# Kernel tuning notes

Measured on AMD Instinct MI355X. Metric: run time of the kernel, lower is better.

Reference implementation:

```python
import jax, jax.numpy as jnp
import numpy as np

H = 12
D_MODEL = 768
D_K = D_MODEL // H  # 64


def setup_inputs() -> dict:
    key = jax.random.key(0)
    ks = jax.random.split(key, 16)
    B, S, D = 4, 1024, D_MODEL
    scale = 1.0 / np.sqrt(D)
    inp = {
        "query": jax.random.normal(ks[0], (B, S, D), jnp.float32),
        "key": jax.random.normal(ks[1], (B, S, D), jnp.float32),
        "value": jax.random.normal(ks[2], (B, S, D), jnp.float32),
        "times": jax.random.normal(ks[3], (2, B, S, D), jnp.float32),
        # learned params (Linear weights stored torch-style [out, in])
        "Wq": jax.random.normal(ks[4], (D, D), jnp.float32) * scale,
        "bq": jnp.zeros((D,), jnp.float32),
        "Wk": jax.random.normal(ks[5], (D, D), jnp.float32) * scale,
        "bk": jnp.zeros((D,), jnp.float32),
        "Wv": jax.random.normal(ks[6], (D, D), jnp.float32) * scale,
        "bv": jnp.zeros((D,), jnp.float32),
        "Wt": jax.random.normal(ks[7], (D, D), jnp.float32) * scale,
        "bt": jnp.zeros((D,), jnp.float32),
        "Wo": jax.random.normal(ks[8], (D, D), jnp.float32) * scale,
        "bo": jnp.zeros((D,), jnp.float32),
    }
    return inp


def _split_heads(x, B, S):
    # [B,S,D] -> [B,H,S,D_K]
    return x.reshape(B, S, H, D_K).transpose(0, 2, 1, 3)


def reference(query, key, value, times, Wq, bq, Wk, bk, Wv, bv, Wt, bt, Wo, bo):
    B, S, D = query.shape
    inv_sqrt_dk = 1.0 / jnp.sqrt(jnp.asarray(D_K, query.dtype))
    # q/k/v projections are identical across time-loop iterations; hoist them.
    q = _split_heads(query @ Wq.T + bq, B, S)   # [B,H,S,dk]
    k = _split_heads(key @ Wk.T + bk, B, S)
    v = _split_heads(value @ Wv.T + bv, B, S)
    x = jnp.zeros_like(q)
    n_times = times.shape[0]
    for i in range(n_times):  # small fixed loop over time embeddings
        t = _split_heads(times[i] @ Wt.T + bt, B, S)
        # dual-score attention: query.time + query.key, each scaled by 1/sqrt(d_k)
        scores = (jnp.einsum('bhqd,bhkd->bhqk', q, t)
                  + jnp.einsum('bhqd,bhkd->bhqk', q, k)) * inv_sqrt_dk
        p = jax.nn.softmax(scores, axis=-1)
        x = x + jnp.einsum('bhqk,bhkd->bhqd', p, v)
    x = x.transpose(0, 2, 1, 3).reshape(B, S, H * D_K)
    return x @ Wo.T + bo
```

## Files before the change

### kernel.cpp

```cpp
#include <hip/hip_runtime.h>
#include <hip/hip_fp16.h>

typedef _Float16 v8h __attribute__((ext_vector_type(8)));
typedef _Float16 v4h __attribute__((ext_vector_type(4)));
typedef float v4f __attribute__((ext_vector_type(4)));

#define MFMA_F16 __builtin_amdgcn_mfma_f32_16x16x32_f16

__device__ static inline void async_copy16(const void* g, void* l) {
  __builtin_amdgcn_global_load_lds(
      (const __attribute__((address_space(1))) void*)g,
      (__attribute__((address_space(3))) void*)l, 16, 0, 0);
}

struct CastArgs {
  const float* src[10];
  _Float16* dst[10];
  int n8[10];
  float scale[10];
};
__global__ void cast_all(CastArgs a) {
  const int z = blockIdx.y;
  const int i = blockIdx.x * 256 + threadIdx.x;
  if (i >= a.n8[z]) return;
  const float sc = a.scale[z];
  const float* s = a.src[z] + (size_t)i * 8;
  const float4 f0 = *(const float4*)s;
  const float4 f1 = *(const float4*)(s + 4);
  v8h o = {(_Float16)(f0.x * sc), (_Float16)(f0.y * sc),
           (_Float16)(f0.z * sc), (_Float16)(f0.w * sc),
           (_Float16)(f1.x * sc), (_Float16)(f1.y * sc),
           (_Float16)(f1.z * sc), (_Float16)(f1.w * sc)};
  *(v8h*)(a.dst[z] + (size_t)i * 8) = o;
}

struct GemmArgs {
  const _Float16* A1[4]; const _Float16* A2[4];
  const _Float16* W1[4]; const _Float16* W2[4];
  const float* b1[4];    const float* b2[4];
  void* out[4];
  float bscale[4];
  int K[4];
  int mode[4];
};

__global__ __launch_bounds__(256) void gemm_mt(GemmArgs g) {
  __shared__ _Float16 a_lds[128 * 64];
  __shared__ _Float16 w_lds[128 * 64];
  const int z = blockIdx.z;
  const int KK = g.K[z];
  const int tid = threadIdx.x;
  const int w = tid >> 6, lane = tid & 63, quad = lane >> 4, l16 = lane & 15;
  const int m0 = blockIdx.x * 128, n0 = blockIdx.y * 128;
  const int wm = (w >> 1) * 64, wn = (w & 1) * 64;

  size_t srcOff[4]; int ldsOff[4];
  #pragma unroll
  for (int i = 0; i < 4; ++i) {
    const int c = i * 256 + tid, row = c >> 3, slot = c & 7;
    srcOff[i] = (size_t)row * 768 + (size_t)((slot ^ (row & 7)) * 8);
    ldsOff[i] = (i * 256 + w * 64) * 8;
  }

  v4f acc[4][4] = {};

  for (int k0 = 0; k0 < KK; k0 += 64) {
    const _Float16* Asrc = (k0 < 768) ? g.A1[z] : g.A2[z];
    const _Float16* Wsrc = (k0 < 768) ? g.W1[z] : g.W2[z];
    const int kc = (k0 < 768) ? k0 : k0 - 768;
    __syncthreads();
    #pragma unroll
    for (int i = 0; i < 4; ++i) {
      async_copy16(Asrc + (size_t)m0 * 768 + kc + srcOff[i], &a_lds[ldsOff[i]]);
      async_copy16(Wsrc + (size_t)n0 * 768 + kc + srcOff[i], &w_lds[ldsOff[i]]);
    }
    __syncthreads();

    #pragma unroll
    for (int kh = 0; kh < 2; ++kh) {
      v8h af[4], bf[4];
      #pragma unroll
      for (int mt = 0; mt < 4; ++mt) {
        const int r = wm + mt * 16 + l16;
        af[mt] = *(const v8h*)&a_lds[r * 64 + (((kh * 4 + quad) ^ (r & 7)) * 8)];
      }
      #pragma unroll
      for (int nt = 0; nt < 4; ++nt) {
        const int r = wn + nt * 16 + l16;
        bf[nt] = *(const v8h*)&w_lds[r * 64 + (((kh * 4 + quad) ^ (r & 7)) * 8)];
      }
      #pragma unroll
      for (int mt = 0; mt < 4; ++mt)
        #pragma unroll
        for (int nt = 0; nt < 4; ++nt)
          acc[mt][nt] = MFMA_F16(af[mt], bf[nt], acc[mt][nt], 0, 0, 0);
    }
  }

  const int mode = g.mode[z];
  #pragma unroll
  for (int nt = 0; nt < 4; ++nt) {
    const int col = n0 + wn + nt * 16 + l16;
    float bv = g.b1[z][col] * g.bscale[z];
    if (g.b2[z]) bv += g.b2[z][col];
    if (mode == 1) {
      _Float16* outp = (_Float16*)g.out[z];
      const int h = col >> 6, dk = col & 63;
      #pragma unroll
      for (int mt = 0; mt < 4; ++mt) {
        const int row = m0 + wm + mt * 16 + quad * 4;
        const int b = row >> 10, s = row & 1023;
        v4h pack = {(_Float16)(acc[mt][nt][0] + bv), (_Float16)(acc[mt][nt][1] + bv),
                    (_Float16)(acc[mt][nt][2] + bv), (_Float16)(acc[mt][nt][3] + bv)};
        *(v4h*)&outp[(size_t)((b * 12 + h) * 64 + dk) * 1024 + s] = pack;
      }
    } else {
      #pragma unroll
      for (int mt = 0; mt < 4; ++mt)
        #pragma unroll
        for (int r = 0; r < 4; ++r) {
          const int row = m0 + wm + mt * 16 + quad * 4 + r;
          const float v = acc[mt][nt][r] + bv;
          if (mode == 2) ((float*)g.out[z])[(size_t)row * 768 + col] = v;
          else ((_Float16*)g.out[z])[(size_t)row * 768 + col] = (_Float16)v;
        }
    }
  }
}

__global__ __launch_bounds__(128) void attn(
    const _Float16* __restrict__ Q,
    const _Float16* __restrict__ KT0, const _Float16* __restrict__ KT1,
    const _Float16* __restrict__ Vt,
    _Float16* __restrict__ X)
{
  __shared__ _Float16 kt0[2][2048];
  __shared__ _Float16 kt1[2][2048];
  __shared__ _Float16 vt[2][2048];
  __shared__ _Float16 p_lds[2][2][2][16 * 40];

  const int tid = threadIdx.x;
  const int w = tid >> 6, lane = tid & 63, quad = lane >> 4, l16 = lane & 15;
  const int bh = blockIdx.y, b = bh / 12, h = bh % 12;
  const int q0 = blockIdx.x * 64;
  const size_t base = (size_t)b * 1024 * 768 + h * 64;

  const _Float16* KT0b = KT0 + base;
  const _Float16* KT1b = KT1 + base;
  const _Float16* Vtb = Vt + (size_t)bh * 64 * 1024;

  size_t ktOff[2], vOff[2]; int ldsOff[2];
  #pragma unroll
  for (int i = 0; i < 2; ++i) {
    const int c = i * 128 + w * 64 + lane, row = c >> 3, slot = c & 7;
    const int logical = slot ^ (row & 7);
    ktOff[i] = (size_t)row * 768 + (size_t)(logical * 8);
    vOff[i] = (size_t)(row * 2 + (logical >> 2)) * 1024 + (size_t)((logical & 3) * 8);
    ldsOff[i] = c * 8;
  }
  auto stage = [&](int kv0, int buf) {
    #pragma unroll
    for (int i = 0; i < 2; ++i) {
      async_copy16(KT0b + (size_t)kv0 * 768 + ktOff[i], &kt0[buf][ldsOff[i]]);
      async_copy16(KT1b + (size_t)kv0 * 768 + ktOff[i], &kt1[buf][ldsOff[i]]);
      async_copy16(Vtb + vOff[i] + kv0, &vt[buf][ldsOff[i]]);
    }
  };

  const _Float16* Qw = Q + base + (size_t)(q0 + w * 32) * 768;
  v8h qf[2][2];
  #pragma unroll
  for (int u = 0; u < 2; ++u)
    #pragma unroll
    for (int kh = 0; kh < 2; ++kh)
      qf[u][kh] = *(const v8h*)(Qw + (size_t)(u * 16 + l16) * 768 + kh * 32 + quad * 8);

  v4f o[2][2][4] = {};
  float sm[2][2][4] = {};

  stage(0, 0);
  for (int c = 0; c < 32; ++c) {
    __syncthreads();
    if (c < 31) stage((c + 1) * 32, (c + 1) & 1);
    const _Float16* k0p = &kt0[c & 1][0];
    const _Float16* k1p = &kt1[c & 1][0];
    const _Float16* vp = &vt[c & 1][0];

    v8h bfr[2][2][2];
    #pragma unroll
    for (int kvt = 0; kvt < 2; ++kvt) {
      const int r = kvt * 16 + l16, rw = r & 7;
      bfr[0][kvt][0] = *(const v8h*)&k0p[r * 64 + ((quad ^ rw) * 8)];
      bfr[0][kvt][1] = *(const v8h*)&k0p[r * 64 + (((4 + quad) ^ rw) * 8)];
      bfr[1][kvt][0] = *(const v8h*)&k1p[r * 64 + ((quad ^ rw) * 8)];
      bfr[1][kvt][1] = *(const v8h*)&k1p[r * 64 + (((4 + quad) ^ rw) * 8)];
    }

    v4f s[2][2][2] = {};
    #pragma unroll
    for (int u = 0; u < 2; ++u)
      #pragma unroll
      for (int t = 0; t < 2; ++t)
        #pragma unroll
        for (int kvt = 0; kvt < 2; ++kvt) {
          s[u][t][kvt] = MFMA_F16(qf[u][0], bfr[t][kvt][0], s[u][t][kvt], 0, 0, 0);
          s[u][t][kvt] = MFMA_F16(qf[u][1], bfr[t][kvt][1], s[u][t][kvt], 0, 0, 0);
        }

    #pragma unroll
    for (int u = 0; u < 2; ++u)
      #pragma unroll
      for (int t = 0; t < 2; ++t) {
        _Float16* pl = &p_lds[w][u][t][0];
        #pragma unroll
        for (int r = 0; r < 4; ++r) {
          const int prow = quad * 4 + r;
          const float e0 = __expf(s[u][t][0][r]);
          const float e1 = __expf(s[u][t][1][r]);
          sm[u][t][r] += e0 + e1;
          pl[prow * 40 + l16] = (_Float16)e0;
          pl[prow * 40 + 16 + l16] = (_Float16)e1;
        }
      }
    __builtin_amdgcn_s_waitcnt(0xC07F);

    v8h pf[2][2];
    #pragma unroll
    for (int u = 0; u < 2; ++u)
      #pragma unroll
      for (int t = 0; t < 2; ++t)
        pf[u][t] = *(const v8h*)&p_lds[w][u][t][l16 * 40 + quad * 8];

    #pragma unroll
    for (int nt = 0; nt < 4; ++nt) {
      const int n = nt * 16 + l16, row = n >> 1;
      const int slot = ((n & 1) * 4 + quad) ^ (row & 7);
      const v8h vf = *(const v8h*)&vp[row * 64 + slot * 8];
      #pragma unroll
      for (int u = 0; u < 2; ++u)
        #pragma unroll
        for (int t = 0; t < 2; ++t)
          o[u][t][nt] = MFMA_F16(pf[u][t], vf, o[u][t][nt], 0, 0, 0);
    }
  }

  #pragma unroll
  for (int u = 0; u < 2; ++u) {
    _Float16* Xw = X + base + (size_t)(q0 + w * 32 + u * 16) * 768;
    #pragma unroll
    for (int r = 0; r < 4; ++r) {
      float s0 = sm[u][0][r], s1 = sm[u][1][r];
      s0 += __shfl_xor(s0, 1); s0 += __shfl_xor(s0, 2);
      s0 += __shfl_xor(s0, 4); s0 += __shfl_xor(s0, 8);
      s1 += __shfl_xor(s1, 1); s1 += __shfl_xor(s1, 2);
      s1 += __shfl_xor(s1, 4); s1 += __shfl_xor(s1, 8);
      const float i0 = 1.0f / s0, i1 = 1.0f / s1;
      #pragma unroll
      for (int nt = 0; nt < 4; ++nt)
        Xw[(size_t)(quad * 4 + r) * 768 + nt * 16 + l16] =
            (_Float16)(o[u][0][nt][r] * i0 + o[u][1][nt][r] * i1);
    }
  }
}

extern "C" void kernel_launch(void* const* d_in, const int* in_sizes, int n_in,
                              void* d_out, int out_size, void* d_ws, size_t ws_size,
                              hipStream_t stream) {
  const float* query = (const float*)d_in[0];
  const float* key   = (const float*)d_in[1];
  const float* value = (const float*)d_in[2];
  const float* times = (const float*)d_in[3];
  const float* Wq = (const float*)d_in[4];  const float* bq = (const float*)d_in[5];
  const float* Wk = (const float*)d_in[6];  const float* bk = (const float*)d_in[7];
  const float* Wv = (const float*)d_in[8];  const float* bv = (const float*)d_in[9];
  const float* Wt = (const float*)d_in[10]; const float* bt = (const float*)d_in[11];
  const float* Wo = (const float*)d_in[12]; const float* bo = (const float*)d_in[13];
  float* out = (float*)d_out;

  const size_t NELEM = (size_t)4096 * 768;
  const size_t WELEM = (size_t)768 * 768;

  char* ws = (char*)d_ws;
  size_t off = 0;
  auto alloc = [&](size_t bytes) {
    void* p = ws + off; off += (bytes + 255) & ~(size_t)255; return p;
  };
  _Float16* qh  = (_Float16*)alloc(NELEM * 2);
  _Float16* kh  = (_Float16*)alloc(NELEM * 2);
  _Float16* vh  = (_Float16*)alloc(NELEM * 2);
  _Float16* wqh = (_Float16*)alloc(WELEM * 2);
  _Float16* wkh = (_Float16*)alloc(WELEM * 2);
  _Float16* wvh = (_Float16*)alloc(WELEM * 2);
  _Float16* wth = (_Float16*)alloc(WELEM * 2);
  _Float16* woh = (_Float16*)alloc(WELEM * 2);
  _Float16* Qh  = (_Float16*)alloc(NELEM * 2);
  _Float16* KT0 = (_Float16*)alloc(NELEM * 2);
  _Float16* KT1 = (_Float16*)alloc(NELEM * 2);
  _Float16* Vt  = (_Float16*)alloc(NELEM * 2);
  _Float16* t0h = (_Float16*)d_out;
  _Float16* t1h = t0h + NELEM;
  _Float16* Xh = qh;

  CastArgs ca = {};
  const int nA8 = (int)(NELEM / 8), nW8 = (int)(WELEM / 8);
  const float* csrc[10] = {query, key, value, times, times + NELEM, Wq, Wk, Wv, Wt, Wo};
  _Float16* cdst[10] = {qh, kh, vh, t0h, t1h, wqh, wkh, wvh, wth, woh};
  for (int i = 0; i < 10; ++i) {
    ca.src[i] = csrc[i]; ca.dst[i] = cdst[i];
    ca.n8[i] = (i < 5) ? nA8 : nW8;
    ca.scale[i] = (i == 5) ? 0.125f : 1.0f;
  }
  cast_all<<<dim3((nA8 + 255) / 256, 10), 256, 0, stream>>>(ca);

  GemmArgs pa = {};
  pa.A1[0] = t0h; pa.A2[0] = kh; pa.W1[0] = wth; pa.W2[0] = wkh;
  pa.b1[0] = bt; pa.b2[0] = bk; pa.out[0] = KT0; pa.bscale[0] = 1.0f;
  pa.K[0] = 1536; pa.mode[0] = 0;
  pa.A1[1] = t1h; pa.A2[1] = kh; pa.W1[1] = wth; pa.W2[1] = wkh;
  pa.b1[1] = bt; pa.b2[1] = bk; pa.out[1] = KT1; pa.bscale[1] = 1.0f;
  pa.K[1] = 1536; pa.mode[1] = 0;
  pa.A1[2] = qh; pa.A2[2] = qh; pa.W1[2] = wqh; pa.W2[2] = wqh;
  pa.b1[2] = bq; pa.b2[2] = nullptr; pa.out[2] = Qh; pa.bscale[2] = 0.125f;
  pa.K[2] = 768; pa.mode[2] = 0;
  pa.A1[3] = vh; pa.A2[3] = vh; pa.W1[3] = wvh; pa.W2[3] = wvh;
  pa.b1[3] = bv; pa.b2[3] = nullptr; pa.out[3] = Vt; pa.bscale[3] = 1.0f;
  pa.K[3] = 768; pa.mode[3] = 1;
  gemm_mt<<<dim3(32, 6, 4), 256, 0, stream>>>(pa);

  attn<<<dim3(16, 48), 128, 0, stream>>>(Qh, KT0, KT1, Vt, Xh);

  GemmArgs oa = {};
  oa.A1[0] = Xh; oa.A2[0] = Xh; oa.W1[0] = woh; oa.W2[0] = woh;
  oa.b1[0] = bo; oa.b2[0] = nullptr; oa.out[0] = out; oa.bscale[0] = 1.0f;
  oa.K[0] = 768; oa.mode[0] = 2;
  gemm_mt<<<dim3(32, 6, 1), 256, 0, stream>>>(oa);
}
```

Measured before the change: 243.0 us.

## Compute transposed scores so softmax probabilities feed PV MFMA directly from registers

```diff
diff --git a/kernel.cpp b/kernel.cpp
--- a/kernel.cpp
+++ b/kernel.cpp
@@ -6,6 +6,7 @@
 typedef float v4f __attribute__((ext_vector_type(4)));
 
 #define MFMA_F16 __builtin_amdgcn_mfma_f32_16x16x32_f16
+#define MFMA16_F16 __builtin_amdgcn_mfma_f32_16x16x16f16
 
 __device__ static inline void async_copy16(const void* g, void* l) {
   __builtin_amdgcn_global_load_lds(
@@ -128,7 +129,7 @@
   }
 }
 
-__global__ __launch_bounds__(128) void attn(
+__global__ __launch_bounds__(256) void attn(
     const _Float16* __restrict__ Q,
     const _Float16* __restrict__ KT0, const _Float16* __restrict__ KT1,
     const _Float16* __restrict__ Vt,
@@ -137,7 +138,6 @@
   __shared__ _Float16 kt0[2][2048];
   __shared__ _Float16 kt1[2][2048];
   __shared__ _Float16 vt[2][2048];
-  __shared__ _Float16 p_lds[2][2][2][16 * 40];
 
   const int tid = threadIdx.x;
   const int w = tid >> 6, lane = tid & 63, quad = lane >> 4, l16 = lane & 15;
@@ -149,117 +149,87 @@
   const _Float16* KT1b = KT1 + base;
   const _Float16* Vtb = Vt + (size_t)bh * 64 * 1024;
 
-  size_t ktOff[2], vOff[2]; int ldsOff[2];
-  #pragma unroll
-  for (int i = 0; i < 2; ++i) {
-    const int c = i * 128 + w * 64 + lane, row = c >> 3, slot = c & 7;
-    const int logical = slot ^ (row & 7);
-    ktOff[i] = (size_t)row * 768 + (size_t)(logical * 8);
-    vOff[i] = (size_t)(row * 2 + (logical >> 2)) * 1024 + (size_t)((logical & 3) * 8);
-    ldsOff[i] = c * 8;
-  }
+  const int c = w * 64 + lane;
+  const int ktRow = c >> 3, ktSlot = c & 7;
+  const size_t ktOff = (size_t)ktRow * 768 + (size_t)((ktSlot ^ (ktRow & 7)) * 8);
+  const int vRow = c >> 2, vSlot = c & 3;
+  const size_t vOff = (size_t)vRow * 1024 + (size_t)((vSlot ^ (vRow & 3)) * 8);
+  const int ldsOff = c * 8;
+
   auto stage = [&](int kv0, int buf) {
-    #pragma unroll
-    for (int i = 0; i < 2; ++i) {
-      async_copy16(KT0b + (size_t)kv0 * 768 + ktOff[i], &kt0[buf][ldsOff[i]]);
-      async_copy16(KT1b + (size_t)kv0 * 768 + ktOff[i], &kt1[buf][ldsOff[i]]);
-      async_copy16(Vtb + vOff[i] + kv0, &vt[buf][ldsOff[i]]);
-    }
+    async_copy16(KT0b + (size_t)kv0 * 768 + ktOff, &kt0[buf][ldsOff]);
+    async_copy16(KT1b + (size_t)kv0 * 768 + ktOff, &kt1[buf][ldsOff]);
+    async_copy16(Vtb + (size_t)kv0 + vOff, &vt[buf][ldsOff]);
   };
 
-  const _Float16* Qw = Q + base + (size_t)(q0 + w * 32) * 768;
-  v8h qf[2][2];
-  #pragma unroll
-  for (int u = 0; u < 2; ++u)
-    #pragma unroll
-    for (int kh = 0; kh < 2; ++kh)
-      qf[u][kh] = *(const v8h*)(Qw + (size_t)(u * 16 + l16) * 768 + kh * 32 + quad * 8);
-
-  v4f o[2][2][4] = {};
-  float sm[2][2][4] = {};
+  const _Float16* Qw = Q + base + (size_t)(q0 + w * 16) * 768;
+  const v8h qf0 = *(const v8h*)(Qw + (size_t)l16 * 768 + quad * 8);
+  const v8h qf1 = *(const v8h*)(Qw + (size_t)l16 * 768 + 32 + quad * 8);
+
+  v4f o[2][4] = {};
+  float lsum[2] = {0.f, 0.f};
 
   stage(0, 0);
-  for (int c = 0; c < 32; ++c) {
+  for (int cc = 0; cc < 32; ++cc) {
     __syncthreads();
-    if (c < 31) stage((c + 1) * 32, (c + 1) & 1);
-    const _Float16* k0p = &kt0[c & 1][0];
-    const _Float16* k1p = &kt1[c & 1][0];
-    const _Float16* vp = &vt[c & 1][0];
-
-    v8h bfr[2][2][2];
+    if (cc < 31) stage((cc + 1) * 32, (cc + 1) & 1);
+    const _Float16* k0p = &kt0[cc & 1][0];
+    const _Float16* k1p = &kt1[cc & 1][0];
+    const _Float16* vp = &vt[cc & 1][0];
+
+    v4f s[2][2] = {};
     #pragma unroll
     for (int kvt = 0; kvt < 2; ++kvt) {
       const int r = kvt * 16 + l16, rw = r & 7;
-      bfr[0][kvt][0] = *(const v8h*)&k0p[r * 64 + ((quad ^ rw) * 8)];
-      bfr[0][kvt][1] = *(const v8h*)&k0p[r * 64 + (((4 + quad) ^ rw) * 8)];
-      bfr[1][kvt][0] = *(const v8h*)&k1p[r * 64 + ((quad ^ rw) * 8)];
-      bfr[1][kvt][1] = *(const v8h*)&k1p[r * 64 + (((4 + quad) ^ rw) * 8)];
-    }
-
-    v4f s[2][2][2] = {};
-    #pragma unroll
-    for (int u = 0; u < 2; ++u)
-      #pragma unroll
-      for (int t = 0; t < 2; ++t)
-        #pragma unroll
-        for (int kvt = 0; kvt < 2; ++kvt) {
-          s[u][t][kvt] = MFMA_F16(qf[u][0], bfr[t][kvt][0], s[u][t][kvt], 0, 0, 0);
-          s[u][t][kvt] = MFMA_F16(qf[u][1], bfr[t][kvt][1], s[u][t][kvt], 0, 0, 0);
-        }
-
-    #pragma unroll
-    for (int u = 0; u < 2; ++u)
-      #pragma unroll
-      for (int t = 0; t < 2; ++t) {
-        _Float16* pl = &p_lds[w][u][t][0];
-        #pragma unroll
-        for (int r = 0; r < 4; ++r) {
-          const int prow = quad * 4 + r;
-          const float e0 = __expf(s[u][t][0][r]);
-          const float e1 = __expf(s[u][t][1][r]);
-          sm[u][t][r] += e0 + e1;
-          pl[prow * 40 + l16] = (_Float16)e0;
-          pl[prow * 40 + 16 + l16] = (_Float16)e1;
-        }
-      }
-    __builtin_amdgcn_s_waitcnt(0xC07F);
-
-    v8h pf[2][2];
-    #pragma unroll
-    for (int u = 0; u < 2; ++u)
-      #pragma unroll
-      for (int t = 0; t < 2; ++t)
-        pf[u][t] = *(const v8h*)&p_lds[w][u][t][l16 * 40 + quad * 8];
-
-    #pragma unroll
-    for (int nt = 0; nt < 4; ++nt) {
-      const int n = nt * 16 + l16, row = n >> 1;
-      const int slot = ((n & 1) * 4 + quad) ^ (row & 7);
-      const v8h vf = *(const v8h*)&vp[row * 64 + slot * 8];
-      #pragma unroll
-      for (int u = 0; u < 2; ++u)
-        #pragma unroll
-        for (int t = 0; t < 2; ++t)
-          o[u][t][nt] = MFMA_F16(pf[u][t], vf, o[u][t][nt], 0, 0, 0);
-    }
-  }
-
+      const v8h k00 = *(const v8h*)&k0p[r * 64 + ((quad ^ rw) * 8)];
+      const v8h k01 = *(const v8h*)&k0p[r * 64 + (((4 + quad) ^ rw) * 8)];
+      const v8h k10 = *(const v8h*)&k1p[r * 64 + ((quad ^ rw) * 8)];
+      const v8h k11 = *(const v8h*)&k1p[r * 64 + (((4 + quad) ^ rw) * 8)];
+      s[0][kvt] = MFMA_F16(k00, qf0, s[0][kvt], 0, 0, 0);
+      s[0][kvt] = MFMA_F16(k01, qf1, s[0][kvt], 0, 0, 0);
+      s[1][kvt] = MFMA_F16(k10, qf0, s[1][kvt], 0, 0, 0);
+      s[1][kvt] = MFMA_F16(k11, qf1, s[1][kvt], 0, 0, 0);
+    }
+
+    v4h pb[2][2];
+    #pragma unroll
+    for (int t = 0; t < 2; ++t)
+      #pragma unroll
+      for (int kvt = 0; kvt < 2; ++kvt) {
+        const float e0 = __expf(s[t][kvt][0]);
+        const float e1 = __expf(s[t][kvt][1]);
+        const float e2 = __expf(s[t][kvt][2]);
+        const float e3 = __expf(s[t][kvt][3]);
+        lsum[t] += (e0 + e1) + (e2 + e3);
+        pb[t][kvt] = v4h{(_Float16)e0, (_Float16)e1, (_Float16)e2, (_Float16)e3};
+      }
+
+    #pragma unroll
+    for (int dkt = 0; dkt < 4; ++dkt) {
+      const int row = dkt * 16 + l16;
+      #pragma unroll
+      for (int kvt = 0; kvt < 2; ++kvt) {
+        const int slot = (kvt * 2 + (quad >> 1)) ^ (row & 3);
+        const v4h vf = *(const v4h*)&vp[row * 32 + slot * 8 + (quad & 1) * 4];
+        o[0][dkt] = MFMA16_F16(vf, pb[0][kvt], o[0][dkt], 0, 0, 0);
+        o[1][dkt] = MFMA16_F16(vf, pb[1][kvt], o[1][dkt], 0, 0, 0);
+      }
+    }
+  }
+
+  float s0 = lsum[0], s1 = lsum[1];
+  s0 += __shfl_xor(s0, 16); s0 += __shfl_xor(s0, 32);
+  s1 += __shfl_xor(s1, 16); s1 += __shfl_xor(s1, 32);
+  const float i0 = 1.0f / s0, i1 = 1.0f / s1;
+
+  _Float16* Xw = X + base + (size_t)(q0 + w * 16 + l16) * 768;
   #pragma unroll
-  for (int u = 0; u < 2; ++u) {
-    _Float16* Xw = X + base + (size_t)(q0 + w * 32 + u * 16) * 768;
-    #pragma unroll
-    for (int r = 0; r < 4; ++r) {
-      float s0 = sm[u][0][r], s1 = sm[u][1][r];
-      s0 += __shfl_xor(s0, 1); s0 += __shfl_xor(s0, 2);
-      s0 += __shfl_xor(s0, 4); s0 += __shfl_xor(s0, 8);
-      s1 += __shfl_xor(s1, 1); s1 += __shfl_xor(s1, 2);
-      s1 += __shfl_xor(s1, 4); s1 += __shfl_xor(s1, 8);
-      const float i0 = 1.0f / s0, i1 = 1.0f / s1;
-      #pragma unroll
-      for (int nt = 0; nt < 4; ++nt)
-        Xw[(size_t)(quad * 4 + r) * 768 + nt * 16 + l16] =
-            (_Float16)(o[u][0][nt][r] * i0 + o[u][1][nt][r] * i1);
-    }
+  for (int dkt = 0; dkt < 4; ++dkt) {
+    v4h pack;
+    #pragma unroll
+    for (int r = 0; r < 4; ++r)
+      pack[r] = (_Float16)(o[0][dkt][r] * i0 + o[1][dkt][r] * i1);
+    *(v4h*)&Xw[dkt * 16 + quad * 4] = pack;
   }
 }
 
@@ -327,7 +297,7 @@
   pa.K[3] = 768; pa.mode[3] = 1;
   gemm_mt<<<dim3(32, 6, 4), 256, 0, stream>>>(pa);
 
-  attn<<<dim3(16, 48), 128, 0, stream>>>(Qh, KT0, KT1, Vt, Xh);
+  attn<<<dim3(16, 48), 256, 0, stream>>>(Qh, KT0, KT1, Vt, Xh);
 
   GemmArgs oa = {};
   oa.A1[0] = Xh; oa.A2[0] = Xh; oa.W1[0] = woh; oa.W2[0] = woh;
```

Result: no change. 240.8 us (-0.9%).
